# Kernel tuning notes

Hardware: AMD Instinct MI355X
Metric: run time of the kernel (lower is better)

The kernel has to match this reference:

```python
import jax, jax.numpy as jnp
import numpy as np

NEG_SLOPE = 0.2  # PyG GATConv default negative_slope


def gat_conv(x, edge_index, W, att_src, att_dst, bias, concat):
    """PyG-style GATConv (eval mode, add_self_loops=True).
    W: [in, H*C]; att_src/att_dst: [H, C]; bias: [H*C] or [C]."""
    N = x.shape[0]
    H, C = att_src.shape
    loop = jnp.arange(N, dtype=edge_index.dtype)
    src = jnp.concatenate([edge_index[0], loop])  # message sources
    dst = jnp.concatenate([edge_index[1], loop])  # aggregation targets
    h = (x @ W).reshape(N, H, C)                  # [N, H, C]
    a_s = jnp.einsum('nhc,hc->nh', h, att_src)    # [N, H]
    a_d = jnp.einsum('nhc,hc->nh', h, att_dst)
    e = jax.nn.leaky_relu(a_s[src] + a_d[dst], NEG_SLOPE)  # [E, H]
    # segment softmax over incoming edges of each destination node
    m = jax.ops.segment_max(e, dst, num_segments=N)
    ex = jnp.exp(e - m[dst])
    denom = jax.ops.segment_sum(ex, dst, num_segments=N)
    alpha = ex / (denom[dst] + 1e-16)             # [E, H]
    out = jax.ops.segment_sum(h[src] * alpha[:, :, None], dst, num_segments=N)
    out = out.reshape(N, H * C) if concat else out.mean(axis=1)
    return out + bias


def setup_inputs() -> dict:
    key = jax.random.key(0)
    ks = jax.random.split(key, 13)
    N, E, G = 100000, 3200000, 512
    IN, HID, HEADS, OUT = 1, 8, 8, 10
    p = lambda k, shape: jax.random.normal(k, shape, jnp.float32) * 0.1
    return {
        'x': jax.random.normal(ks[0], (N, IN), jnp.float32),
        'edge_index': jax.random.randint(ks[1], (2, E), 0, N),
        'batch': jnp.sort(jax.random.randint(ks[2], (N,), 0, G)),
        'num_graphs': G,
        'W1': p(ks[3], (IN, HEADS * HID)),
        'att_src1': p(ks[4], (HEADS, HID)),
        'att_dst1': p(ks[5], (HEADS, HID)),
        'b1': jnp.zeros((HEADS * HID,), jnp.float32),
        'W2': p(ks[6], (HEADS * HID, HID)),
        'att_src2': p(ks[7], (1, HID)),
        'att_dst2': p(ks[8], (1, HID)),
        'b2': jnp.zeros((HID,), jnp.float32),
        'lin_w': p(ks[9], (HID, OUT)),
        'lin_b': jnp.zeros((OUT,), jnp.float32),
    }


def reference(x, edge_index, batch, num_graphs, W1, att_src1, att_dst1, b1,
              W2, att_src2, att_dst2, b2, lin_w, lin_b):
    # eval mode: F.dropout is identity
    h = gat_conv(x, edge_index, W1, att_src1, att_dst1, b1, concat=True)   # [N, 64]
    h = jax.nn.elu(h)
    h = gat_conv(h, edge_index, W2, att_src2, att_dst2, b2, concat=False)  # [N, 8]
    # global mean pool over graphs
    sums = jax.ops.segment_sum(h, batch, num_segments=num_graphs)
    cnt = jax.ops.segment_sum(jnp.ones((h.shape[0], 1), h.dtype), batch,
                              num_segments=num_graphs)
    pooled = sums / jnp.maximum(cnt, 1.0)                                   # [G, 8]
    logits = pooled @ lin_w + lin_b                                         # [G, 10]
    return jax.nn.log_softmax(logits, axis=1)
```

## Files before the change

kernel.cpp:

```cpp
#include <hip/hip_runtime.h>
#include <hip/hip_bf16.h>

#define NEG 0.2f
#define NBMAX 512
#define BCAP 12288
#define TILE 8192

__global__ void __launch_bounds__(512) kP_bucket(
    const int* __restrict__ src, const int* __restrict__ dst,
    int* __restrict__ gcur, unsigned int* __restrict__ packed, int E, int NB)
{
    __shared__ int hist[NBMAX], lofs[NBMAX], gbase[NBMAX], cur[NBMAX], s[NBMAX];
    __shared__ unsigned int stage[TILE];
    int tid = threadIdx.x;
    hist[tid] = 0;
    __syncthreads();
    int t0 = blockIdx.x * TILE;
    int tend = t0 + TILE; if (tend > E) tend = E;
    for (int i = t0 + tid; i < tend; i += 512)
        atomicAdd(&hist[dst[i] >> 8], 1);
    __syncthreads();
    int v = hist[tid];
    s[tid] = v;
    __syncthreads();
    for (int off = 1; off < NBMAX; off <<= 1) {
        int t = (tid >= off) ? s[tid - off] : 0;
        __syncthreads();
        s[tid] += t;
        __syncthreads();
    }
    lofs[tid] = s[tid] - v;
    gbase[tid] = v ? atomicAdd(&gcur[tid], v) : 0;
    cur[tid] = 0;
    __syncthreads();
    for (int i = t0 + tid; i < tend; i += 512) {
        int d = dst[i];
        int j = d >> 8;
        int pos = lofs[j] + atomicAdd(&cur[j], 1);
        stage[pos] = ((unsigned)src[i] << 8) | (unsigned)(d & 255);
    }
    __syncthreads();
    int wave = tid >> 6, lane = tid & 63;
    for (int j = wave; j < NB; j += 8) {
        int h = hist[j], lo = lofs[j], gb = gbase[j];
        for (int k = lane; k < h; k += 64) {
            int gp = gb + k;
            if (gp < BCAP) packed[(size_t)j * BCAP + gp] = stage[lo + k];
        }
    }
}

__global__ void __launch_bounds__(512) kL1(
    const int* __restrict__ gcur, unsigned int* packed,
    const float* __restrict__ x,
    const float* __restrict__ W1, const float* __restrict__ as1, const float* __restrict__ ad1,
    const float* __restrict__ b1, const float* __restrict__ W2,
    const float* __restrict__ as2w, const float* __restrict__ ad2w,
    int* __restrict__ rowS, int* __restrict__ rowE,
    float* __restrict__ h2, float* __restrict__ as2, float* __restrict__ ad2, int N)
{
    __shared__ int hist[256], roff[256], cur[256];
    __shared__ int stage[BCAP];
    __shared__ float S1[8], D1[8], sW1[64], sb1[64], sW2[512], sas[8], sad[8];
    int tid = threadIdx.x, b = blockIdx.x;
    if (tid < 8) {
        float sv = 0.f, dv = 0.f;
        for (int c = 0; c < 8; ++c) {
            float w = W1[tid * 8 + c];
            sv += w * as1[tid * 8 + c];
            dv += w * ad1[tid * 8 + c];
        }
        S1[tid] = sv; D1[tid] = dv;
        sas[tid] = as2w[tid]; sad[tid] = ad2w[tid];
    }
    for (int i = tid; i < 64; i += 512) { sW1[i] = W1[i]; sb1[i] = b1[i]; }
    if (tid < 512) sW2[tid] = W2[tid];
    if (tid < 256) hist[tid] = 0;
    __syncthreads();
    int cnt = gcur[b]; if (cnt > BCAP) cnt = BCAP;
    size_t base = (size_t)b * BCAP;
    unsigned int* pk = packed + base;
    for (int i = tid; i < cnt; i += 512)
        atomicAdd(&hist[pk[i] & 255], 1);
    __syncthreads();
    int v = (tid < 256) ? hist[tid] : 0;
    if (tid < 256) roff[tid] = v;
    __syncthreads();
    for (int off = 1; off < 256; off <<= 1) {
        int t = (tid >= off && tid < 256) ? roff[tid - off] : 0;
        __syncthreads();
        if (tid < 256) roff[tid] += t;
        __syncthreads();
    }
    if (tid < 256) cur[tid] = roff[tid] - v;
    __syncthreads();
    for (int i = tid; i < cnt; i += 512) {
        unsigned p = pk[i];
        int pos = atomicAdd(&cur[p & 255], 1);
        stage[pos] = (int)(p >> 8);
    }
    __syncthreads();
    for (int i = tid; i < cnt; i += 512)
        pk[i] = (unsigned)stage[i];
    int nl = tid >> 1, sub = tid & 1;
    int node = b * 256 + nl;
    bool valid = node < N;
    int end = roff[nl], start = end - hist[nl];
    if (valid && sub == 0) { rowS[node] = (int)base + start; rowE[node] = (int)base + end; }
    float xdv = valid ? x[node] : 0.f;
    float s1r[8], d1r[8];
    #pragma unroll
    for (int h = 0; h < 8; ++h) { s1r[h] = S1[h]; d1r[h] = D1[h]; }
    float num[8] = {0,0,0,0,0,0,0,0}, den[8] = {0,0,0,0,0,0,0,0};
    if (valid && sub == 0) {
        #pragma unroll
        for (int h = 0; h < 8; ++h) {
            float e = xdv * (s1r[h] + d1r[h]);
            e = fmaxf(e, NEG * e);
            float w = __expf(e);
            den[h] = w; num[h] = w * xdv;
        }
    }
    for (int j = start + sub; j < end; j += 2) {
        float xsv = x[stage[j]];
        #pragma unroll
        for (int h = 0; h < 8; ++h) {
            float e = xsv * s1r[h] + xdv * d1r[h];
            e = fmaxf(e, NEG * e);
            float w = __expf(e);
            den[h] += w; num[h] += w * xsv;
        }
    }
    #pragma unroll
    for (int h = 0; h < 8; ++h) {
        den[h] += __shfl_xor(den[h], 1, 64);
        num[h] += __shfl_xor(num[h], 1, 64);
    }
    if (!valid || sub) return;
    float o[8] = {0,0,0,0,0,0,0,0};
    #pragma unroll
    for (int h = 0; h < 8; ++h) {
        float agg = num[h] / (den[h] + 1e-16f);
        #pragma unroll
        for (int c = 0; c < 8; ++c) {
            float vv = agg * sW1[h * 8 + c] + sb1[h * 8 + c];
            vv = vv > 0.f ? vv : (__expf(vv) - 1.f);
            #pragma unroll
            for (int c2 = 0; c2 < 8; ++c2) o[c2] += vv * sW2[(h * 8 + c) * 8 + c2];
        }
    }
    float as_ = 0.f, ad_ = 0.f;
    #pragma unroll
    for (int c = 0; c < 8; ++c) {
        as_ += o[c] * sas[c];
        ad_ += o[c] * sad[c];
        h2[(size_t)node * 8 + c] = o[c];
    }
    as2[node] = as_; ad2[node] = ad_;
}

__global__ void __launch_bounds__(256) kG2_gather(
    const int* __restrict__ rowS, const int* __restrict__ rowE,
    const unsigned int* __restrict__ csr,
    const float* __restrict__ as2, const float* __restrict__ ad2,
    const float* __restrict__ h2,
    float* __restrict__ out2, int N)
{
    int t = blockIdx.x * blockDim.x + threadIdx.x;
    int node = t >> 3, lane = t & 7;
    if (node >= N) return;
    float add = ad2[node];
    float den = 0.f, num[8] = {0,0,0,0,0,0,0,0};
    if (lane == 0) {
        float e = as2[node] + add;
        e = fmaxf(e, NEG * e);
        float w = __expf(e);
        den = w;
        const float4* hp = (const float4*)&h2[(size_t)node * 8];
        float4 a = hp[0], b = hp[1];
        num[0] = w * a.x; num[1] = w * a.y; num[2] = w * a.z; num[3] = w * a.w;
        num[4] = w * b.x; num[5] = w * b.y; num[6] = w * b.z; num[7] = w * b.w;
    }
    int start = rowS[node], end = rowE[node];
    for (int j = start + lane; j < end; j += 8) {
        int s = (int)csr[j];
        float e = as2[s] + add;
        e = fmaxf(e, NEG * e);
        float w = __expf(e);
        den += w;
        const float4* hp = (const float4*)&h2[(size_t)s * 8];
        float4 a = hp[0], b = hp[1];
        num[0] += w * a.x; num[1] += w * a.y; num[2] += w * a.z; num[3] += w * a.w;
        num[4] += w * b.x; num[5] += w * b.y; num[6] += w * b.z; num[7] += w * b.w;
    }
    #pragma unroll
    for (int off = 4; off >= 1; off >>= 1) {
        den += __shfl_down(den, off, 8);
        #pragma unroll
        for (int c = 0; c < 8; ++c) num[c] += __shfl_down(num[c], off, 8);
    }
    if (lane == 0) {
        float dv = den + 1e-16f;
        #pragma unroll
        for (int c = 0; c < 8; ++c) out2[(size_t)node * 8 + c] = num[c] / dv;
    }
}

__global__ void __launch_bounds__(256) kB_starts(
    const int* __restrict__ batch, int* __restrict__ gstart, int N, int G)
{
    int n = blockIdx.x * blockDim.x + threadIdx.x;
    if (n >= N) return;
    int b0 = batch[n];
    if (n == 0) {
        for (int g = 0; g <= b0; ++g) gstart[g] = 0;
    } else {
        int bp = batch[n - 1];
        for (int g = bp + 1; g <= b0; ++g) gstart[g] = n;
    }
    if (n == N - 1) {
        for (int g = b0 + 1; g <= G; ++g) gstart[g] = N;
    }
}

__global__ void __launch_bounds__(256) kPool(
    const float* __restrict__ out2, const int* __restrict__ gstart,
    const float* __restrict__ b2v,
    const float* __restrict__ lin_w, const float* __restrict__ lin_b,
    float* __restrict__ out, int G)
{
    __shared__ float sw[80], sb[10], sb2[8];
    if (threadIdx.x < 80) sw[threadIdx.x] = lin_w[threadIdx.x];
    if (threadIdx.x < 10) sb[threadIdx.x] = lin_b[threadIdx.x];
    if (threadIdx.x < 8)  sb2[threadIdx.x] = b2v[threadIdx.x];
    __syncthreads();
    int wid = (blockIdx.x * blockDim.x + threadIdx.x) >> 6;
    if (wid >= G) return;
    int lane = threadIdx.x & 63;
    int ch = lane & 7, sub = lane >> 3;
    int start = gstart[wid], end = gstart[wid + 1];
    int cntn = end - start;
    float acc = 0.f;
    for (int i = start + sub; i < end; i += 8)
        acc += out2[(size_t)i * 8 + ch];
    acc += __shfl_down(acc, 32, 64);
    acc += __shfl_down(acc, 16, 64);
    acc += __shfl_down(acc, 8, 64);
    float inv = (cntn > 0) ? 1.f / (float)cntn : 0.f;
    float p[8];
    #pragma unroll
    for (int i = 0; i < 8; ++i) {
        float tt = __shfl(acc, i, 64);
        p[i] = (cntn > 0) ? (tt * inv + sb2[i]) : 0.f;
    }
    float l[10]; float m = -1e30f;
    #pragma unroll
    for (int j = 0; j < 10; ++j) {
        float v = sb[j];
        #pragma unroll
        for (int i = 0; i < 8; ++i) v += p[i] * sw[i * 10 + j];
        l[j] = v; m = v > m ? v : m;
    }
    float sum = 0.f;
    #pragma unroll
    for (int j = 0; j < 10; ++j) sum += __expf(l[j] - m);
    float lse = m + __logf(sum);
    if (lane < 10) out[(size_t)wid * 10 + lane] = l[lane] - lse;
}

extern "C" void kernel_launch(void* const* d_in, const int* in_sizes, int n_in,
                              void* d_out, int out_size, void* d_ws, size_t ws_size,
                              hipStream_t stream) {
    const float* x    = (const float*)d_in[0];
    const int*   ei   = (const int*)d_in[1];
    const int*   batch= (const int*)d_in[2];
    const float* W1   = (const float*)d_in[4];
    const float* as1  = (const float*)d_in[5];
    const float* ad1  = (const float*)d_in[6];
    const float* b1   = (const float*)d_in[7];
    const float* W2   = (const float*)d_in[8];
    const float* as2w = (const float*)d_in[9];
    const float* ad2w = (const float*)d_in[10];
    const float* b2v  = (const float*)d_in[11];
    const float* lw   = (const float*)d_in[12];
    const float* lb   = (const float*)d_in[13];
    float* out = (float*)d_out;

    const int N = in_sizes[0];
    const int E = in_sizes[1] / 2;
    const int G = out_size / 10;
    const int* srcI = ei;
    const int* dstI = ei + E;
    const int NB = (N + 255) >> 8;

    int*   gcur = (int*)d_ws;
    unsigned int* packed = (unsigned int*)(gcur + 512);
    int*   rowS = (int*)(packed + (size_t)NB * BCAP);
    int*   rowE = rowS + N;
    float* h2   = (float*)(rowE + N);
    float* as2  = h2 + (size_t)8 * N;
    float* ad2  = as2 + N;
    float* out2 = ad2 + N;
    int*   gstart = (int*)(out2 + (size_t)8 * N);

    const int B = 256;
    hipMemsetAsync(gcur, 0, 512 * sizeof(int), stream);

    kP_bucket<<<(E + TILE - 1) / TILE, 512, 0, stream>>>(srcI, dstI, gcur, packed, E, NB);
    kB_starts<<<(N + B - 1) / B, B, 0, stream>>>(batch, gstart, N, G);
    kL1<<<NB, 512, 0, stream>>>(gcur, packed, x, W1, as1, ad1, b1, W2, as2w, ad2w,
                                rowS, rowE, h2, as2, ad2, N);
    kG2_gather<<<(N * 8 + B - 1) / B, B, 0, stream>>>(rowS, rowE, packed, as2, ad2, h2,
                                                      out2, N);
    kPool<<<(G * 64 + B - 1) / B, B, 0, stream>>>(out2, gstart, b2v, lw, lb, out, G);
}
```

Measured before the change: 213.9 us.

## Shrink dst buckets to 64 nodes and cache dst in registers during bucketing

Destination buckets shrink from 256 to 64 nodes, which gives about 1563 buckets of capacity 3328, and the bucketing tile grows to 12500 edges held in registers across both passes. The block scans become wave-shuffle prefix sums, and the scatter gives each bucket a 16-lane subgroup. kL1 now runs 256 threads per 64-node bucket with 4 lanes per node, so there are more blocks and more parallelism per node. The tradeoffs are many more global atomics on gcur per tile and more, shorter scatter segments, and buckets can overflow if the degree skew is high.

```diff
diff --git a/kernel.cpp b/kernel.cpp
--- a/kernel.cpp
+++ b/kernel.cpp
@@ -2,55 +2,83 @@
 #include <hip/hip_bf16.h>
 
 #define NEG 0.2f
-#define NBMAX 512
-#define BCAP 12288
-#define TILE 8192
+#define NBC 1568
+#define BCAP 3328
+#define TILE 12500
+#define EPT 25
 
 __global__ void __launch_bounds__(512) kP_bucket(
     const int* __restrict__ src, const int* __restrict__ dst,
     int* __restrict__ gcur, unsigned int* __restrict__ packed, int E, int NB)
 {
-    __shared__ int hist[NBMAX], lofs[NBMAX], gbase[NBMAX], cur[NBMAX], s[NBMAX];
+    __shared__ int hist[NBC], lofs[NBC], gbase[NBC], cur[NBC];
+    __shared__ int wtot[8], wpre[8];
     __shared__ unsigned int stage[TILE];
     int tid = threadIdx.x;
-    hist[tid] = 0;
+    int lane = tid & 63, wv = tid >> 6;
+    for (int j = tid; j < NBC; j += 512) hist[j] = 0;
     __syncthreads();
     int t0 = blockIdx.x * TILE;
     int tend = t0 + TILE; if (tend > E) tend = E;
-    for (int i = t0 + tid; i < tend; i += 512)
-        atomicAdd(&hist[dst[i] >> 8], 1);
-    __syncthreads();
-    int v = hist[tid];
-    s[tid] = v;
-    __syncthreads();
-    for (int off = 1; off < NBMAX; off <<= 1) {
-        int t = (tid >= off) ? s[tid - off] : 0;
-        __syncthreads();
-        s[tid] += t;
-        __syncthreads();
-    }
-    lofs[tid] = s[tid] - v;
-    gbase[tid] = v ? atomicAdd(&gcur[tid], v) : 0;
-    cur[tid] = 0;
-    __syncthreads();
-    for (int i = t0 + tid; i < tend; i += 512) {
-        int d = dst[i];
-        int j = d >> 8;
-        int pos = lofs[j] + atomicAdd(&cur[j], 1);
-        stage[pos] = ((unsigned)src[i] << 8) | (unsigned)(d & 255);
-    }
-    __syncthreads();
-    int wave = tid >> 6, lane = tid & 63;
-    for (int j = wave; j < NB; j += 8) {
-        int h = hist[j], lo = lofs[j], gb = gbase[j];
-        for (int k = lane; k < h; k += 64) {
+    int dreg[EPT];
+    #pragma unroll
+    for (int k = 0; k < EPT; ++k) {
+        int i = t0 + tid + (k << 9);
+        int d = -1;
+        if (i < tend) { d = dst[i]; atomicAdd(&hist[d >> 6], 1); }
+        dreg[k] = d;
+    }
+    __syncthreads();
+    int e0 = 0, e1 = 0, e2 = 0, e3 = 0, idx0 = 4 * tid;
+    if (idx0 < NBC) { e0 = hist[idx0]; e1 = hist[idx0+1]; e2 = hist[idx0+2]; e3 = hist[idx0+3]; }
+    int ssum = e0 + e1 + e2 + e3;
+    int incl = ssum;
+    #pragma unroll
+    for (int off = 1; off < 64; off <<= 1) {
+        int t = __shfl_up(incl, off, 64);
+        if (lane >= off) incl += t;
+    }
+    if (lane == 63) wtot[wv] = incl;
+    __syncthreads();
+    if (tid == 0) { int p = 0; for (int i = 0; i < 8; ++i) { wpre[i] = p; p += wtot[i]; } }
+    __syncthreads();
+    if (idx0 < NBC) {
+        int base = wpre[wv] + incl - ssum;
+        lofs[idx0] = base;         base += e0;
+        lofs[idx0+1] = base;       base += e1;
+        lofs[idx0+2] = base;       base += e2;
+        lofs[idx0+3] = base;
+    }
+    for (int j = tid; j < NBC; j += 512) {
+        int h = hist[j];
+        gbase[j] = h ? atomicAdd(&gcur[j], h) : 0;
+        cur[j] = 0;
+    }
+    __syncthreads();
+    #pragma unroll
+    for (int k = 0; k < EPT; ++k) {
+        int d = dreg[k];
+        if (d >= 0) {
+            int i = t0 + tid + (k << 9);
+            int j = d >> 6;
+            int pos = lofs[j] + atomicAdd(&cur[j], 1);
+            stage[pos] = ((unsigned)src[i] << 6) | (unsigned)(d & 63);
+        }
+    }
+    __syncthreads();
+    int sg = lane >> 4, sl = lane & 15;
+    for (int j = wv * 4 + sg; j < NB; j += 32) {
+        int h = hist[j];
+        if (!h) continue;
+        int lo = lofs[j], gb = gbase[j];
+        for (int k = sl; k < h; k += 16) {
             int gp = gb + k;
             if (gp < BCAP) packed[(size_t)j * BCAP + gp] = stage[lo + k];
         }
     }
 }
 
-__global__ void __launch_bounds__(512) kL1(
+__global__ void __launch_bounds__(256) kL1(
     const int* __restrict__ gcur, unsigned int* packed,
     const float* __restrict__ x,
     const float* __restrict__ W1, const float* __restrict__ as1, const float* __restrict__ ad1,
@@ -59,7 +87,7 @@
     int* __restrict__ rowS, int* __restrict__ rowE,
     float* __restrict__ h2, float* __restrict__ as2, float* __restrict__ ad2, int N)
 {
-    __shared__ int hist[256], roff[256], cur[256];
+    __shared__ int hist[64], roff[64], cur[64];
     __shared__ int stage[BCAP];
     __shared__ float S1[8], D1[8], sW1[64], sb1[64], sW2[512], sas[8], sad[8];
     int tid = threadIdx.x, b = blockIdx.x;
@@ -73,40 +101,40 @@
         S1[tid] = sv; D1[tid] = dv;
         sas[tid] = as2w[tid]; sad[tid] = ad2w[tid];
     }
-    for (int i = tid; i < 64; i += 512) { sW1[i] = W1[i]; sb1[i] = b1[i]; }
-    if (tid < 512) sW2[tid] = W2[tid];
-    if (tid < 256) hist[tid] = 0;
+    if (tid < 64) { sW1[tid] = W1[tid]; sb1[tid] = b1[tid]; hist[tid] = 0; }
+    sW2[tid] = W2[tid]; sW2[tid + 256] = W2[tid + 256];
     __syncthreads();
     int cnt = gcur[b]; if (cnt > BCAP) cnt = BCAP;
     size_t base = (size_t)b * BCAP;
     unsigned int* pk = packed + base;
-    for (int i = tid; i < cnt; i += 512)
-        atomicAdd(&hist[pk[i] & 255], 1);
-    __syncthreads();
-    int v = (tid < 256) ? hist[tid] : 0;
-    if (tid < 256) roff[tid] = v;
-    __syncthreads();
-    for (int off = 1; off < 256; off <<= 1) {
-        int t = (tid >= off && tid < 256) ? roff[tid - off] : 0;
-        __syncthreads();
-        if (tid < 256) roff[tid] += t;
-        __syncthreads();
-    }
-    if (tid < 256) cur[tid] = roff[tid] - v;
-    __syncthreads();
-    for (int i = tid; i < cnt; i += 512) {
+    for (int i = tid; i < cnt; i += 256)
+        atomicAdd(&hist[pk[i] & 63], 1);
+    __syncthreads();
+    if (tid < 64) {
+        int v = hist[tid];
+        int s = v;
+        #pragma unroll
+        for (int off = 1; off < 64; off <<= 1) {
+            int t = __shfl_up(s, off, 64);
+            if (tid >= off) s += t;
+        }
+        roff[tid] = s;
+        cur[tid] = s - v;
+    }
+    __syncthreads();
+    for (int i = tid; i < cnt; i += 256) {
         unsigned p = pk[i];
-        int pos = atomicAdd(&cur[p & 255], 1);
-        stage[pos] = (int)(p >> 8);
-    }
-    __syncthreads();
-    for (int i = tid; i < cnt; i += 512)
+        int pos = atomicAdd(&cur[p & 63], 1);
+        stage[pos] = (int)(p >> 6);
+    }
+    __syncthreads();
+    for (int i = tid; i < cnt; i += 256)
         pk[i] = (unsigned)stage[i];
-    int nl = tid >> 1, sub = tid & 1;
-    int node = b * 256 + nl;
+    int nl = tid >> 2, sub = tid & 3;
+    int node = b * 64 + nl;
     bool valid = node < N;
-    int end = roff[nl], start = end - hist[nl];
-    if (valid && sub == 0) { rowS[node] = (int)base + start; rowE[node] = (int)base + end; }
+    int en = roff[nl], st = en - hist[nl];
+    if (valid && sub == 0) { rowS[node] = (int)base + st; rowE[node] = (int)base + en; }
     float xdv = valid ? x[node] : 0.f;
     float s1r[8], d1r[8];
     #pragma unroll
@@ -121,7 +149,7 @@
             den[h] = w; num[h] = w * xdv;
         }
     }
-    for (int j = start + sub; j < end; j += 2) {
+    for (int j = st + sub; j < en; j += 4) {
         float xsv = x[stage[j]];
         #pragma unroll
         for (int h = 0; h < 8; ++h) {
@@ -135,6 +163,8 @@
     for (int h = 0; h < 8; ++h) {
         den[h] += __shfl_xor(den[h], 1, 64);
         num[h] += __shfl_xor(num[h], 1, 64);
+        den[h] += __shfl_xor(den[h], 2, 64);
+        num[h] += __shfl_xor(num[h], 2, 64);
     }
     if (!valid || sub) return;
     float o[8] = {0,0,0,0,0,0,0,0};
@@ -291,11 +321,11 @@
     const int G = out_size / 10;
     const int* srcI = ei;
     const int* dstI = ei + E;
-    const int NB = (N + 255) >> 8;
+    const int NB = (N + 63) >> 6;
 
     int*   gcur = (int*)d_ws;
-    unsigned int* packed = (unsigned int*)(gcur + 512);
-    int*   rowS = (int*)(packed + (size_t)NB * BCAP);
+    unsigned int* packed = (unsigned int*)(gcur + 2048);
+    int*   rowS = (int*)(packed + (size_t)NBC * BCAP);
     int*   rowE = rowS + N;
     float* h2   = (float*)(rowE + N);
     float* as2  = h2 + (size_t)8 * N;
@@ -304,12 +334,12 @@
     int*   gstart = (int*)(out2 + (size_t)8 * N);
 
     const int B = 256;
-    hipMemsetAsync(gcur, 0, 512 * sizeof(int), stream);
+    hipMemsetAsync(gcur, 0, 2048 * sizeof(int), stream);
 
     kP_bucket<<<(E + TILE - 1) / TILE, 512, 0, stream>>>(srcI, dstI, gcur, packed, E, NB);
     kB_starts<<<(N + B - 1) / B, B, 0, stream>>>(batch, gstart, N, G);
-    kL1<<<NB, 512, 0, stream>>>(gcur, packed, x, W1, as1, ad1, b1, W2, as2w, ad2w,
-                                rowS, rowE, h2, as2, ad2, N);
+    kL1<<<NB, B, 0, stream>>>(gcur, packed, x, W1, as1, ad1, b1, W2, as2w, ad2w,
+                              rowS, rowE, h2, as2, ad2, N);
     kG2_gather<<<(N * 8 + B - 1) / B, B, 0, stream>>>(rowS, rowE, packed, as2, ad2, h2,
                                                       out2, N);
     kPool<<<(G * 64 + B - 1) / B, B, 0, stream>>>(out2, gstart, b2v, lw, lb, out, G);
```

Result: no change. 218.1 us (+2.0%).

## Restructure bucketing kernel with 1024 threads, register-cached dst and wave-shuffle scan

Applied to the files above, without the earlier changes.

The bucketing kernel now runs 1024-thread blocks over larger tiles (12500 edges) and keeps each thread's dst values in registers, so dst is read from global memory once instead of twice. The 512-entry block scan moves from a shared-memory loop with many barriers to a wave-level shuffle scan plus a small cross-wave prefix. The flush stage uses half-waves per bucket and skips empty buckets. The graph-start computation is folded into kL1, which removes one kernel launch. In exchange there are fewer blocks (256), higher register pressure, and larger per-block shared staging, which may lower occupancy.

```diff
diff --git a/kernel.cpp b/kernel.cpp
--- a/kernel.cpp
+++ b/kernel.cpp
@@ -4,46 +4,65 @@
 #define NEG 0.2f
 #define NBMAX 512
 #define BCAP 12288
-#define TILE 8192
-
-__global__ void __launch_bounds__(512) kP_bucket(
+#define TILE 12500
+#define EPT 13
+
+__global__ void __launch_bounds__(1024) kP_bucket(
     const int* __restrict__ src, const int* __restrict__ dst,
     int* __restrict__ gcur, unsigned int* __restrict__ packed, int E, int NB)
 {
-    __shared__ int hist[NBMAX], lofs[NBMAX], gbase[NBMAX], cur[NBMAX], s[NBMAX];
+    __shared__ int hist[NBMAX], lofs[NBMAX], gbase[NBMAX], cur[NBMAX];
+    __shared__ int wtot[8], wpre[8];
     __shared__ unsigned int stage[TILE];
     int tid = threadIdx.x;
-    hist[tid] = 0;
+    int lane = tid & 63, wv = tid >> 6;
+    if (tid < NBMAX) hist[tid] = 0;
     __syncthreads();
     int t0 = blockIdx.x * TILE;
     int tend = t0 + TILE; if (tend > E) tend = E;
-    for (int i = t0 + tid; i < tend; i += 512)
-        atomicAdd(&hist[dst[i] >> 8], 1);
-    __syncthreads();
-    int v = hist[tid];
-    s[tid] = v;
-    __syncthreads();
-    for (int off = 1; off < NBMAX; off <<= 1) {
-        int t = (tid >= off) ? s[tid - off] : 0;
-        __syncthreads();
-        s[tid] += t;
-        __syncthreads();
-    }
-    lofs[tid] = s[tid] - v;
-    gbase[tid] = v ? atomicAdd(&gcur[tid], v) : 0;
-    cur[tid] = 0;
-    __syncthreads();
-    for (int i = t0 + tid; i < tend; i += 512) {
-        int d = dst[i];
-        int j = d >> 8;
-        int pos = lofs[j] + atomicAdd(&cur[j], 1);
-        stage[pos] = ((unsigned)src[i] << 8) | (unsigned)(d & 255);
-    }
-    __syncthreads();
-    int wave = tid >> 6, lane = tid & 63;
-    for (int j = wave; j < NB; j += 8) {
-        int h = hist[j], lo = lofs[j], gb = gbase[j];
-        for (int k = lane; k < h; k += 64) {
+    int dreg[EPT];
+    #pragma unroll
+    for (int k = 0; k < EPT; ++k) {
+        int i = t0 + tid + (k << 10);
+        int d = -1;
+        if (i < tend) { d = dst[i]; atomicAdd(&hist[d >> 8], 1); }
+        dreg[k] = d;
+    }
+    __syncthreads();
+    int v = (tid < NBMAX) ? hist[tid] : 0;
+    int incl = v;
+    #pragma unroll
+    for (int off = 1; off < 64; off <<= 1) {
+        int t = __shfl_up(incl, off, 64);
+        if (lane >= off) incl += t;
+    }
+    if (tid < NBMAX && lane == 63) wtot[wv] = incl;
+    __syncthreads();
+    if (tid == 0) { int p = 0; for (int i = 0; i < 8; ++i) { wpre[i] = p; p += wtot[i]; } }
+    __syncthreads();
+    if (tid < NBMAX) {
+        lofs[tid] = wpre[wv] + incl - v;
+        gbase[tid] = v ? atomicAdd(&gcur[tid], v) : 0;
+        cur[tid] = 0;
+    }
+    __syncthreads();
+    #pragma unroll
+    for (int k = 0; k < EPT; ++k) {
+        int d = dreg[k];
+        if (d >= 0) {
+            int i = t0 + tid + (k << 10);
+            int j = d >> 8;
+            int pos = lofs[j] + atomicAdd(&cur[j], 1);
+            stage[pos] = ((unsigned)src[i] << 8) | (unsigned)(d & 255);
+        }
+    }
+    __syncthreads();
+    int sg = lane >> 5, sl = lane & 31;
+    for (int j = wv * 2 + sg; j < NB; j += 32) {
+        int h = hist[j];
+        if (!h) continue;
+        int lo = lofs[j], gb = gbase[j];
+        for (int k = sl; k < h; k += 32) {
             int gp = gb + k;
             if (gp < BCAP) packed[(size_t)j * BCAP + gp] = stage[lo + k];
         }
@@ -56,8 +75,9 @@
     const float* __restrict__ W1, const float* __restrict__ as1, const float* __restrict__ ad1,
     const float* __restrict__ b1, const float* __restrict__ W2,
     const float* __restrict__ as2w, const float* __restrict__ ad2w,
+    const int* __restrict__ batch, int* __restrict__ gstart,
     int* __restrict__ rowS, int* __restrict__ rowE,
-    float* __restrict__ h2, float* __restrict__ as2, float* __restrict__ ad2, int N)
+    float* __restrict__ h2, float* __restrict__ as2, float* __restrict__ ad2, int N, int G)
 {
     __shared__ int hist[256], roff[256], cur[256];
     __shared__ int stage[BCAP];
@@ -76,6 +96,15 @@
     for (int i = tid; i < 64; i += 512) { sW1[i] = W1[i]; sb1[i] = b1[i]; }
     if (tid < 512) sW2[tid] = W2[tid];
     if (tid < 256) hist[tid] = 0;
+    if (tid < 256) {
+        int node = b * 256 + tid;
+        if (node < N) {
+            int b0 = batch[node];
+            if (node == 0) { for (int g = 0; g <= b0; ++g) gstart[g] = 0; }
+            else { int bp = batch[node - 1]; for (int g = bp + 1; g <= b0; ++g) gstart[g] = node; }
+            if (node == N - 1) { for (int g = b0 + 1; g <= G; ++g) gstart[g] = N; }
+        }
+    }
     __syncthreads();
     int cnt = gcur[b]; if (cnt > BCAP) cnt = BCAP;
     size_t base = (size_t)b * BCAP;
@@ -105,8 +134,8 @@
     int nl = tid >> 1, sub = tid & 1;
     int node = b * 256 + nl;
     bool valid = node < N;
-    int end = roff[nl], start = end - hist[nl];
-    if (valid && sub == 0) { rowS[node] = (int)base + start; rowE[node] = (int)base + end; }
+    int en = roff[nl], st = en - hist[nl];
+    if (valid && sub == 0) { rowS[node] = (int)base + st; rowE[node] = (int)base + en; }
     float xdv = valid ? x[node] : 0.f;
     float s1r[8], d1r[8];
     #pragma unroll
@@ -121,7 +150,7 @@
             den[h] = w; num[h] = w * xdv;
         }
     }
-    for (int j = start + sub; j < end; j += 2) {
+    for (int j = st + sub; j < en; j += 2) {
         float xsv = x[stage[j]];
         #pragma unroll
         for (int h = 0; h < 8; ++h) {
@@ -206,23 +235,6 @@
     }
 }
 
-__global__ void __launch_bounds__(256) kB_starts(
-    const int* __restrict__ batch, int* __restrict__ gstart, int N, int G)
-{
-    int n = blockIdx.x * blockDim.x + threadIdx.x;
-    if (n >= N) return;
-    int b0 = batch[n];
-    if (n == 0) {
-        for (int g = 0; g <= b0; ++g) gstart[g] = 0;
-    } else {
-        int bp = batch[n - 1];
-        for (int g = bp + 1; g <= b0; ++g) gstart[g] = n;
-    }
-    if (n == N - 1) {
-        for (int g = b0 + 1; g <= G; ++g) gstart[g] = N;
-    }
-}
-
 __global__ void __launch_bounds__(256) kPool(
     const float* __restrict__ out2, const int* __restrict__ gstart,
     const float* __restrict__ b2v,
@@ -306,10 +318,9 @@
     const int B = 256;
     hipMemsetAsync(gcur, 0, 512 * sizeof(int), stream);
 
-    kP_bucket<<<(E + TILE - 1) / TILE, 512, 0, stream>>>(srcI, dstI, gcur, packed, E, NB);
-    kB_starts<<<(N + B - 1) / B, B, 0, stream>>>(batch, gstart, N, G);
+    kP_bucket<<<(E + TILE - 1) / TILE, 1024, 0, stream>>>(srcI, dstI, gcur, packed, E, NB);
     kL1<<<NB, 512, 0, stream>>>(gcur, packed, x, W1, as1, ad1, b1, W2, as2w, ad2w,
-                                rowS, rowE, h2, as2, ad2, N);
+                                batch, gstart, rowS, rowE, h2, as2, ad2, N, G);
     kG2_gather<<<(N * 8 + B - 1) / B, B, 0, stream>>>(rowS, rowE, packed, as2, ad2, h2,
                                                       out2, N);
     kPool<<<(G * 64 + B - 1) / B, B, 0, stream>>>(out2, gstart, b2v, lw, lb, out, G);
```

Result: faster. 199.2 us (-6.9%).
